# Kernel optimization log

Hardware: AMD Instinct MI355X
Metric: run time of the kernel (lower is better)

## Reference

```python
import jax, jax.numpy as jnp
import numpy as np

CHEB_K = 2  # chebyshev polynomial order (support_ks = [I, A] for cheb_k=2)


def _fc(x, w1, b1, w2, b2, w3, b3):
    # FC module: Linear -> sigmoid -> Linear -> sigmoid -> Linear
    h = jax.nn.sigmoid(x @ w1 + b1)
    h = jax.nn.sigmoid(h @ w2 + b2)
    return h @ w3 + b3


def _preprocess(adj):
    # adj: [B,N,N]; add self-loops then row-normalize
    adj = adj + jnp.eye(adj.shape[-1], dtype=adj.dtype)
    return adj / adj.sum(-1, keepdims=True)


def _gcn(x, adjs, ne, wpool, bpool):
    # x: [B,N,C], adjs: list of [B,N,N], ne: [N,E]
    # wpool: [E, 2*CHEB_K, C, O], bpool: [E, O]
    mats = []
    for A in adjs:
        ks = [jnp.broadcast_to(jnp.eye(A.shape[-1], dtype=A.dtype), A.shape), A]
        for _ in range(2, CHEB_K):
            ks.append(2.0 * jnp.matmul(A, ks[-1]) - ks[-2])
        mats.extend(ks)
    # [B,N,K,C] with K = 2*CHEB_K
    x_g = jnp.stack([jnp.einsum('bnm,bmc->bnc', S, x) for S in mats], axis=2)
    weights = jnp.einsum('nd,dkio->nkio', ne, wpool)  # [N,K,C,O]
    bias = ne @ bpool  # [N,O]
    return jnp.einsum('bnki,nkio->bno', x_g, weights) + bias


def _forward(x, state, ne0, ne1, ne2, fc1_w1, fc1_b1, fc1_w2, fc1_b2, fc1_w3, fc1_b3,
             fc2_w1, fc2_b1, fc2_w2, fc2_b2, fc2_w3, fc2_b3, gate_w, gate_b, upd_w, upd_b):
    hid = upd_w.shape[-1]
    ins = jnp.concatenate([x, state], axis=-1)  # [B,N,dim_in+hid]
    f1 = _fc(ins, fc1_w1, fc1_b1, fc1_w2, fc1_b2, fc1_w3, fc1_b3)  # [B,N,TD]
    f2 = _fc(ins, fc2_w1, fc2_b1, fc2_w2, fc2_b2, fc2_w3, fc2_b3)
    nv1 = jnp.tanh(ne0[:, None, :] * f1)  # einsum 'bd,bnd->bnd' == broadcast mul
    nv2 = jnp.tanh(ne1[:, None, :] * f2)
    adj = jnp.einsum('bnd,bmd->bnm', nv1, nv2) - jnp.einsum('bnd,bmd->bnm', nv2, nv1)
    adj1 = _preprocess(jax.nn.relu(adj))
    adj2 = _preprocess(jax.nn.relu(-jnp.swapaxes(adj, -2, -1)))
    z_r = jax.nn.sigmoid(_gcn(ins, [adj1, adj2], ne2, gate_w, gate_b))
    z, r = z_r[..., :hid], z_r[..., hid:]
    cand = jnp.concatenate([x, z * state], axis=-1)
    hc = jnp.tanh(_gcn(cand, [adj1, adj2], ne2, upd_w, upd_b))
    return r * state + (1.0 - r) * hc


def setup_inputs():
    B, N, DIN, DOUT, ED, TD = 32, 1024, 2, 64, 10, 32
    HG, MID = 16, 2  # hyperGNN_dim, middle_dim hardcoded in FC
    CIN = DIN + DOUT
    K2 = 2 * CHEB_K
    ks = jax.random.split(jax.random.key(0), 16)
    rn = lambda i, shape, s=1.0: jax.random.normal(ks[i], shape, dtype=jnp.float32) * s
    return {
        'x': rn(0, (B, N, DIN)),
        'state': rn(1, (B, N, DOUT)),
        'ne0': rn(2, (B, TD)),
        'ne1': rn(3, (B, TD)),
        'ne2': rn(4, (N, ED), 0.1),
        'fc1_w1': rn(5, (CIN, HG), 0.1), 'fc1_b1': jnp.zeros((HG,), jnp.float32),
        'fc1_w2': rn(6, (HG, MID), 0.1), 'fc1_b2': jnp.zeros((MID,), jnp.float32),
        'fc1_w3': rn(7, (MID, TD), 0.1), 'fc1_b3': jnp.zeros((TD,), jnp.float32),
        'fc2_w1': rn(8, (CIN, HG), 0.1), 'fc2_b1': jnp.zeros((HG,), jnp.float32),
        'fc2_w2': rn(9, (HG, MID), 0.1), 'fc2_b2': jnp.zeros((MID,), jnp.float32),
        'fc2_w3': rn(10, (MID, TD), 0.1), 'fc2_b3': jnp.zeros((TD,), jnp.float32),
        'gate_w': rn(11, (ED, K2, CIN, 2 * DOUT), 0.1),
        'gate_b': rn(12, (ED, 2 * DOUT), 0.1),
        'upd_w': rn(13, (ED, K2, CIN, DOUT), 0.1),
        'upd_b': rn(14, (ED, DOUT), 0.1),
    }


def reference(x, state, ne0, ne1, ne2, fc1_w1, fc1_b1, fc1_w2, fc1_b2, fc1_w3, fc1_b3,
              fc2_w1, fc2_b1, fc2_w2, fc2_b2, fc2_w3, fc2_b3, gate_w, gate_b, upd_w, upd_b):
    return _forward(x, state, ne0, ne1, ne2, fc1_w1, fc1_b1, fc1_w2, fc1_b2, fc1_w3, fc1_b3,
                    fc2_w1, fc2_b1, fc2_w2, fc2_b2, fc2_w3, fc2_b3, gate_w, gate_b, upd_w, upd_b)
```

## Files before the change

kernel.cpp:

```cpp
#include <hip/hip_runtime.h>
#include <math.h>

#define BB   32
#define NN   1024
#define DIN  2
#define DOUT 64
#define CIN  66
#define TD   32
#define ED   10
#define OG   128
#define OU   64
#define KP   160
#define XTR  80
#define PS   88

typedef __bf16 bf16x8 __attribute__((ext_vector_type(8)));
typedef float  f32x4  __attribute__((ext_vector_type(4)));
typedef short  s16x8  __attribute__((ext_vector_type(8)));

__device__ __forceinline__ unsigned short f2b(float f) {
    __bf16 h = (__bf16)f;
    return *(unsigned short*)&h;
}

__global__ __launch_bounds__(256) void k_pre(
    const float* __restrict__ x, const float* __restrict__ state,
    const float* __restrict__ ne0, const float* __restrict__ ne1,
    const float* __restrict__ ne2,
    const float* __restrict__ w11, const float* __restrict__ b11,
    const float* __restrict__ w12, const float* __restrict__ b12,
    const float* __restrict__ w13, const float* __restrict__ b13,
    const float* __restrict__ w21, const float* __restrict__ b21,
    const float* __restrict__ w22, const float* __restrict__ b22,
    const float* __restrict__ w23, const float* __restrict__ b23,
    const float* __restrict__ gate_w, const float* __restrict__ gate_b,
    const float* __restrict__ upd_w, const float* __restrict__ upd_b,
    unsigned short* __restrict__ nv1b, unsigned short* __restrict__ nv2b,
    unsigned short* __restrict__ XT0, unsigned short* __restrict__ XT1,
    unsigned short* __restrict__ BcTg, unsigned short* __restrict__ BcTu,
    float* __restrict__ biasG, float* __restrict__ biasU)
{
    __shared__ float sw[2408];
    __shared__ unsigned short st[68*72];
    int blk = blockIdx.x;
    int t = threadIdx.x;

    if (blk < 128) {
        const int oW1 = 0, oB1 = 1056, oW2 = 1072, oB2 = 1104, oW3 = 1108, oB3 = 1172, F2 = 1204;
        for (int i = t; i < 1056; i += 256) { sw[oW1+i] = w11[i]; sw[F2+oW1+i] = w21[i]; }
        if (t < 16) { sw[oB1+t] = b11[t]; sw[F2+oB1+t] = b21[t]; }
        if (t < 32) { sw[oW2+t] = w12[t]; sw[F2+oW2+t] = w22[t]; }
        if (t < 2)  { sw[oB2+t] = b12[t]; sw[F2+oB2+t] = b22[t]; }
        if (t < 64) { sw[oW3+t] = w13[t]; sw[F2+oW3+t] = w23[t]; }
        if (t >= 64 && t < 96) { sw[oB3+t-64] = b13[t-64]; sw[F2+oB3+t-64] = b23[t-64]; }
        __syncthreads();

        int p = blk*256 + t;
        int b = p >> 10;

        float h1a[16], h1b[16];
        #pragma unroll
        for (int j = 0; j < 16; ++j) { h1a[j] = sw[oB1+j]; h1b[j] = sw[F2+oB1+j]; }
        for (int i = 0; i < CIN; ++i) {
            float v = (i < DIN) ? x[(size_t)p*DIN + i] : state[(size_t)p*DOUT + (i-DIN)];
            #pragma unroll
            for (int jq = 0; jq < 4; ++jq) {
                float4 wa = *(const float4*)&sw[oW1 + i*16 + jq*4];
                float4 wb = *(const float4*)&sw[F2 + oW1 + i*16 + jq*4];
                h1a[jq*4+0] += v*wa.x; h1a[jq*4+1] += v*wa.y;
                h1a[jq*4+2] += v*wa.z; h1a[jq*4+3] += v*wa.w;
                h1b[jq*4+0] += v*wb.x; h1b[jq*4+1] += v*wb.y;
                h1b[jq*4+2] += v*wb.z; h1b[jq*4+3] += v*wb.w;
            }
        }
        #pragma unroll
        for (int j = 0; j < 16; ++j) {
            h1a[j] = 1.f/(1.f + __expf(-h1a[j]));
            h1b[j] = 1.f/(1.f + __expf(-h1b[j]));
        }
        float h2a0 = sw[oB2+0], h2a1 = sw[oB2+1];
        float h2b0 = sw[F2+oB2+0], h2b1 = sw[F2+oB2+1];
        #pragma unroll
        for (int i = 0; i < 16; ++i) {
            h2a0 += h1a[i]*sw[oW2 + i*2 + 0];
            h2a1 += h1a[i]*sw[oW2 + i*2 + 1];
            h2b0 += h1b[i]*sw[F2+oW2 + i*2 + 0];
            h2b1 += h1b[i]*sw[F2+oW2 + i*2 + 1];
        }
        h2a0 = 1.f/(1.f + __expf(-h2a0)); h2a1 = 1.f/(1.f + __expf(-h2a1));
        h2b0 = 1.f/(1.f + __expf(-h2b0)); h2b1 = 1.f/(1.f + __expf(-h2b1));

        const float* pn0 = ne0 + b*TD;
        const float* pn1 = ne1 + b*TD;
        #pragma unroll
        for (int jq = 0; jq < 8; ++jq) {
            float4 ba  = *(const float4*)&sw[oB3 + jq*4];
            float4 wa0 = *(const float4*)&sw[oW3 + jq*4];
            float4 wa1 = *(const float4*)&sw[oW3 + 32 + jq*4];
            float4 bb2 = *(const float4*)&sw[F2+oB3 + jq*4];
            float4 wb0 = *(const float4*)&sw[F2+oW3 + jq*4];
            float4 wb1 = *(const float4*)&sw[F2+oW3 + 32 + jq*4];
            float4 n0 = *(const float4*)&pn0[jq*4];
            float4 n1 = *(const float4*)&pn1[jq*4];
            ushort4 u1, u2;
            u1.x = f2b(tanhf(n0.x*(ba.x + h2a0*wa0.x + h2a1*wa1.x)));
            u1.y = f2b(tanhf(n0.y*(ba.y + h2a0*wa0.y + h2a1*wa1.y)));
            u1.z = f2b(tanhf(n0.z*(ba.z + h2a0*wa0.z + h2a1*wa1.z)));
            u1.w = f2b(tanhf(n0.w*(ba.w + h2a0*wa0.w + h2a1*wa1.w)));
            u2.x = f2b(tanhf(n1.x*(bb2.x + h2b0*wb0.x + h2b1*wb1.x)));
            u2.y = f2b(tanhf(n1.y*(bb2.y + h2b0*wb0.y + h2b1*wb1.y)));
            u2.z = f2b(tanhf(n1.z*(bb2.z + h2b0*wb0.z + h2b1*wb1.z)));
            u2.w = f2b(tanhf(n1.w*(bb2.w + h2b0*wb0.w + h2b1*wb1.w)));
            *(ushort4*)&nv1b[(size_t)p*TD + jq*4] = u1;
            *(ushort4*)&nv2b[(size_t)p*TD + jq*4] = u2;
        }
    } else if (blk < 640) {
        int idx = blk - 128;
        int b = idx >> 4, m0 = (idx & 15)*64;
        for (int i = t; i < 1024; i += 256) {
            int m = i >> 4, cq = i & 15;
            size_t base = (size_t)b*NN + m0 + m;
            float4 v = *(const float4*)&state[base*DOUT + cq*4];
            st[(2 + cq*4 + 0)*72 + m] = f2b(v.x);
            st[(2 + cq*4 + 1)*72 + m] = f2b(v.y);
            st[(2 + cq*4 + 2)*72 + m] = f2b(v.z);
            st[(2 + cq*4 + 3)*72 + m] = f2b(v.w);
        }
        if (t < 128) {
            int m = t >> 1, c = t & 1;
            st[c*72 + m] = f2b(x[((size_t)b*NN + m0 + m)*DIN + c]);
        }
        __syncthreads();
        const unsigned int ONE2 = 0x3F803F80u;
        for (int i = t; i < XTR*8; i += 256) {
            int c = i >> 3, ch = i & 7;
            uint4 v;
            if (c < 66)      v = *(const uint4*)&st[c*72 + ch*8];
            else if (c == 66) v = make_uint4(ONE2, ONE2, ONE2, ONE2);
            else              v = make_uint4(0, 0, 0, 0);
            *(uint4*)&XT0[((size_t)b*XTR + c)*NN + m0 + ch*8] = v;
            if (c < 2 || c >= 66)
                *(uint4*)&XT1[((size_t)b*XTR + c)*NN + m0 + ch*8] = v;
        }
    } else if (blk < 1840) {
        int tid = (blk - 640)*256 + t;
        int c = tid / KP, k = tid - c*KP;
        const float* pool; int O, cc; unsigned short* dst;
        if (c < 1280) { pool = gate_w; O = OG; cc = c;        dst = BcTg; }
        else          { pool = upd_w;  O = OU; cc = c - 1280; dst = BcTu; }
        int d = cc / O, o = cc - d*O;
        float v = 0.f;
        if (k < 132) {
            int kp = (k < 66) ? 0 : 1;
            int i  = (k < 66) ? k : k - 66;
            v = pool[(size_t)((d*4 + kp)*CIN + i)*O + o]
              + pool[(size_t)((d*4 + kp + 2)*CIN + i)*O + o];
        }
        dst[(size_t)cc*KP + k] = f2b(v);
    } else {
        int i = (blk - 1840)*256 + t;
        int n = i / 192, j = i - n*192;
        float v = 0.f;
        if (j < 128) {
            #pragma unroll
            for (int d = 0; d < ED; ++d) v += ne2[(size_t)n*ED + d]*gate_b[d*OG + j];
            biasG[(size_t)n*OG + j] = v;
        } else {
            int o = j - 128;
            #pragma unroll
            for (int d = 0; d < ED; ++d) v += ne2[(size_t)n*ED + d]*upd_b[d*OU + o];
            biasU[(size_t)n*OU + o] = v;
        }
    }
}

__global__ __launch_bounds__(256) void k_aapply(
    const unsigned short* __restrict__ nv1b, const unsigned short* __restrict__ nv2b,
    const unsigned short* __restrict__ XTg, unsigned short* __restrict__ A)
{
    __shared__ unsigned short s_nv1r[64*40], s_nv2r[64*40];
    __shared__ unsigned short s_nv1c[64*40], s_nv2c[64*40];
    __shared__ unsigned short s_p[64*PS];
    __shared__ unsigned short s_xt[80*72];
    __shared__ float s_rs[64];

    int t = threadIdx.x;
    int id = blockIdx.x;
    int b = id & 31, rbase = (id >> 5)*64;
    int w = t >> 6, lane = t & 63, lq = lane >> 4, ln = lane & 15;

    for (int i = t; i < 512; i += 256) {
        int arr = i >> 8, j = i & 255;
        int node = j >> 2, ch = j & 3;
        const unsigned short* src = (arr ? nv2b : nv1b)
            + ((size_t)b*NN + rbase + node)*TD + ch*8;
        unsigned short* dst = (arr ? s_nv2r : s_nv1r) + node*40 + ch*8;
        *(uint4*)dst = *(const uint4*)src;
    }
    __syncthreads();

    bf16x8 a1 = *(const bf16x8*)&s_nv1r[(16*w + ln)*40 + lq*8];
    s16x8 a2s = *(const s16x8*)&s_nv2r[(16*w + ln)*40 + lq*8];
    const s16x8 sgn = {(short)0x8000,(short)0x8000,(short)0x8000,(short)0x8000,
                       (short)0x8000,(short)0x8000,(short)0x8000,(short)0x8000};
    a2s ^= sgn;
    bf16x8 a2n = (bf16x8)a2s;

    f32x4 acc[5];
    #pragma unroll
    for (int i = 0; i < 5; ++i) acc[i] = (f32x4){0.f,0.f,0.f,0.f};
    const f32x4 zero4 = {0.f,0.f,0.f,0.f};

    for (int mb = 0; mb < NN; mb += 64) {
        __syncthreads();
        for (int i = t; i < 512; i += 256) {
            int arr = i >> 8, j = i & 255;
            int node = j >> 2, ch = j & 3;
            const unsigned short* src = (arr ? nv2b : nv1b)
                + ((size_t)b*NN + mb + node)*TD + ch*8;
            unsigned short* dst = (arr ? s_nv2c : s_nv1c) + node*40 + ch*8;
            *(uint4*)dst = *(const uint4*)src;
        }
        for (int i = t; i < 640; i += 256) {
            int c = i >> 3, ch = i & 7;
            *(uint4*)&s_xt[c*72 + ch*8] =
                *(const uint4*)&XTg[((size_t)b*XTR + c)*NN + mb + ch*8];
        }
        __syncthreads();

        #pragma unroll
        for (int j0t = 0; j0t < 4; ++j0t) {
            int j0 = j0t*16;
            bf16x8 b2 = *(const bf16x8*)&s_nv2c[(j0 + ln)*40 + lq*8];
            bf16x8 b1 = *(const bf16x8*)&s_nv1c[(j0 + ln)*40 + lq*8];
            f32x4 s = __builtin_amdgcn_mfma_f32_16x16x32_bf16(a1,  b2, zero4, 0, 0, 0);
            s       = __builtin_amdgcn_mfma_f32_16x16x32_bf16(a2n, b1, s,     0, 0, 0);
            #pragma unroll
            for (int r = 0; r < 4; ++r) {
                float p = fmaxf(s[r], 0.f);
                *(__bf16*)&s_p[(16*w + lq*4 + r)*PS + j0 + ln] = (__bf16)p;
            }
        }

        bf16x8 pa0 = *(const bf16x8*)&s_p[(16*w + ln)*PS +      lq*8];
        bf16x8 pa1 = *(const bf16x8*)&s_p[(16*w + ln)*PS + 32 + lq*8];
        #pragma unroll
        for (int n0t = 0; n0t < 5; ++n0t) {
            int n0 = n0t*16;
            bf16x8 xb0 = *(const bf16x8*)&s_xt[(n0 + ln)*72 +      lq*8];
            bf16x8 xb1 = *(const bf16x8*)&s_xt[(n0 + ln)*72 + 32 + lq*8];
            acc[n0t] = __builtin_amdgcn_mfma_f32_16x16x32_bf16(pa0, xb0, acc[n0t], 0, 0, 0);
            acc[n0t] = __builtin_amdgcn_mfma_f32_16x16x32_bf16(pa1, xb1, acc[n0t], 0, 0, 0);
        }
    }

    if (ln == 2) {
        #pragma unroll
        for (int r = 0; r < 4; ++r) s_rs[16*w + lq*4 + r] = acc[4][r];
    }
    float rinv[4];
    #pragma unroll
    for (int r = 0; r < 4; ++r) rinv[r] = 1.0f / (1.0f + s_rs[16*w + lq*4 + r]);

    #pragma unroll
    for (int n0t = 0; n0t < 5; ++n0t) {
        int c = n0t*16 + ln;
        if (c < CIN) {
            #pragma unroll
            for (int r = 0; r < 4; ++r) {
                int gr = rbase + 16*w + lq*4 + r;
                size_t rowG = (size_t)b*NN + gr;
                unsigned short xu = XTg[((size_t)b*XTR + c)*NN + gr];
                float xr = (float)(*(const __bf16*)&xu);
                A[rowG*KP + c]      = xu;
                A[rowG*KP + 66 + c] = f2b((acc[n0t][r] + xr) * rinv[r]);
            }
        }
    }
    for (int i = t; i < 64*28; i += 256) {
        int rr = i / 28, cc = 132 + (i - 28*(i/28));
        A[((size_t)b*NN + rbase + rr)*KP + cc] = 0;
    }
}

template<int O, int MODE>
__global__ __launch_bounds__(256) void k_gemm(
    const unsigned short* __restrict__ A, const unsigned short* __restrict__ BcT,
    const float* __restrict__ ne2, const float* __restrict__ biasP,
    const float* __restrict__ state, unsigned short* __restrict__ XT1,
    float* __restrict__ rbuf, float* __restrict__ out)
{
    __shared__ unsigned short s_b[80*168];

    int t = threadIdx.x;
    int w = t >> 6, lane = t & 63, lq = lane >> 4, ln = lane & 15;
    int o0 = blockIdx.y*16;
    int rowBlock = blockIdx.x*128;
    int rowW = rowBlock + w*32;

    f32x4 acc[2][2][5];
    #pragma unroll
    for (int h = 0; h < 2; ++h)
        #pragma unroll
        for (int f = 0; f < 2; ++f)
            #pragma unroll
            for (int c = 0; c < 5; ++c) acc[h][f][c] = (f32x4){0.f,0.f,0.f,0.f};

    #pragma unroll
    for (int h = 0; h < 2; ++h) {
        if (h) __syncthreads();
        for (int i = t; i < 1600; i += 256) {
            int cc = i / 20, kc = i - cc*20;
            int d = h*5 + (cc >> 4), oo = cc & 15;
            *(uint4*)&s_b[cc*168 + kc*8] =
                *(const uint4*)&BcT[(size_t)(d*O + o0 + oo)*KP + kc*8];
        }
        __syncthreads();

        #pragma unroll
        for (int kc = 0; kc < 5; ++kc) {
            bf16x8 af0 = *(const bf16x8*)&A[(size_t)(rowW      + ln)*KP + kc*32 + lq*8];
            bf16x8 af1 = *(const bf16x8*)&A[(size_t)(rowW + 16 + ln)*KP + kc*32 + lq*8];
            #pragma unroll
            for (int ct = 0; ct < 5; ++ct) {
                bf16x8 bf = *(const bf16x8*)&s_b[(ct*16 + ln)*168 + kc*32 + lq*8];
                acc[h][0][ct] = __builtin_amdgcn_mfma_f32_16x16x32_bf16(af0, bf, acc[h][0][ct], 0, 0, 0);
                acc[h][1][ct] = __builtin_amdgcn_mfma_f32_16x16x32_bf16(af1, bf, acc[h][1][ct], 0, 0, 0);
            }
        }
    }

    int o = o0 + ln;
    #pragma unroll
    for (int f = 0; f < 2; ++f) {
        #pragma unroll
        for (int r = 0; r < 4; ++r) {
            int row_l = w*32 + 16*f + lq*4 + r;
            size_t rowG = (size_t)rowBlock + row_l;
            int n = (int)(rowG & (NN - 1));
            int bb = (int)(rowG >> 10);
            const float* nep = &ne2[(size_t)n*ED];
            float val = biasP[(size_t)n*O + o];
            #pragma unroll
            for (int d = 0; d < 5; ++d) val += nep[d]     * acc[0][f][d][r];
            #pragma unroll
            for (int d = 0; d < 5; ++d) val += nep[5 + d] * acc[1][f][d][r];
            if (MODE == 0) {
                float sv = 1.f/(1.f + __expf(-val));
                if (o0 < 64) {
                    float zst = sv * state[rowG*DOUT + o];
                    XT1[((size_t)bb*XTR + 2 + o)*NN + n] = f2b(zst);
                } else {
                    rbuf[rowG*DOUT + (o - 64)] = sv;
                }
            } else {
                float hc = tanhf(val);
                float rg = rbuf[rowG*DOUT + o];
                float st = state[rowG*DOUT + o];
                out[rowG*DOUT + o] = rg*st + (1.f - rg)*hc;
            }
        }
    }
}

extern "C" void kernel_launch(void* const* d_in, const int* in_sizes, int n_in,
                              void* d_out, int out_size, void* d_ws, size_t ws_size,
                              hipStream_t stream)
{
    const float* x      = (const float*)d_in[0];
    const float* state  = (const float*)d_in[1];
    const float* ne0    = (const float*)d_in[2];
    const float* ne1    = (const float*)d_in[3];
    const float* ne2    = (const float*)d_in[4];
    const float* f1w1   = (const float*)d_in[5];
    const float* f1b1   = (const float*)d_in[6];
    const float* f1w2   = (const float*)d_in[7];
    const float* f1b2   = (const float*)d_in[8];
    const float* f1w3   = (const float*)d_in[9];
    const float* f1b3   = (const float*)d_in[10];
    const float* f2w1   = (const float*)d_in[11];
    const float* f2b1   = (const float*)d_in[12];
    const float* f2w2   = (const float*)d_in[13];
    const float* f2b2   = (const float*)d_in[14];
    const float* f2w3   = (const float*)d_in[15];
    const float* f2b3   = (const float*)d_in[16];
    const float* gate_w = (const float*)d_in[17];
    const float* gate_b = (const float*)d_in[18];
    const float* upd_w  = (const float*)d_in[19];
    const float* upd_b  = (const float*)d_in[20];

    unsigned short* nv1b = (unsigned short*)d_ws;
    unsigned short* nv2b = nv1b + (size_t)BB*NN*TD;
    unsigned short* XT0  = nv2b + (size_t)BB*NN*TD;
    unsigned short* XT1  = XT0  + (size_t)BB*XTR*NN;
    unsigned short* A    = XT1  + (size_t)BB*XTR*NN;
    unsigned short* BcTg = A    + (size_t)BB*NN*KP;
    unsigned short* BcTu = BcTg + (size_t)1280*KP;
    float* biasG = (float*)(BcTu + (size_t)640*KP);
    float* biasU = biasG + (size_t)NN*OG;
    float* rbuf  = biasU + (size_t)NN*OU;
    float* out   = (float*)d_out;

    k_pre<<<dim3(2608), 256, 0, stream>>>(x, state, ne0, ne1, ne2,
        f1w1, f1b1, f1w2, f1b2, f1w3, f1b3,
        f2w1, f2b1, f2w2, f2b2, f2w3, f2b3,
        gate_w, gate_b, upd_w, upd_b,
        nv1b, nv2b, XT0, XT1, BcTg, BcTu, biasG, biasU);

    k_aapply<<<dim3(512), 256, 0, stream>>>(nv1b, nv2b, XT0, A);

    k_gemm<OG,0><<<dim3(BB*NN/128, 8), 256, 0, stream>>>(A, BcTg, ne2, biasG,
                                                         state, XT1, rbuf, nullptr);

    k_aapply<<<dim3(512), 256, 0, stream>>>(nv1b, nv2b, XT1, A);

    k_gemm<OU,1><<<dim3(BB*NN/128, 4), 256, 0, stream>>>(A, BcTu, ne2, biasU,
                                                         state, nullptr, rbuf, out);
}
```

Before: 255.0 us.

## Split k_aapply work across 8 waves with 512-thread blocks

Doubles the block size of the adjacency-apply kernel to 512 threads. Pairs of waves share a 16-row group: each wave computes half of the score tiles, and after a barrier each takes a subset of the output column tiles (3 or 2). This is meant to raise parallelism and latency hiding with only 512 blocks on the device, at the cost of an extra __syncthreads per iteration and unbalanced MFMA work between the two waves of a pair.

```diff
diff --git a/kernel.cpp b/kernel.cpp
--- a/kernel.cpp
+++ b/kernel.cpp
@@ -174,7 +174,7 @@
     }
 }
 
-__global__ __launch_bounds__(256) void k_aapply(
+__global__ __launch_bounds__(512) void k_aapply(
     const unsigned short* __restrict__ nv1b, const unsigned short* __restrict__ nv2b,
     const unsigned short* __restrict__ XTg, unsigned short* __restrict__ A)
 {
@@ -188,9 +188,10 @@
     int id = blockIdx.x;
     int b = id & 31, rbase = (id >> 5)*64;
     int w = t >> 6, lane = t & 63, lq = lane >> 4, ln = lane & 15;
-
-    for (int i = t; i < 512; i += 256) {
-        int arr = i >> 8, j = i & 255;
+    int g = w >> 1, sub = w & 1;
+
+    {
+        int arr = t >> 8, j = t & 255;
         int node = j >> 2, ch = j & 3;
         const unsigned short* src = (arr ? nv2b : nv1b)
             + ((size_t)b*NN + rbase + node)*TD + ch*8;
@@ -199,29 +200,29 @@
     }
     __syncthreads();
 
-    bf16x8 a1 = *(const bf16x8*)&s_nv1r[(16*w + ln)*40 + lq*8];
-    s16x8 a2s = *(const s16x8*)&s_nv2r[(16*w + ln)*40 + lq*8];
+    bf16x8 a1 = *(const bf16x8*)&s_nv1r[(16*g + ln)*40 + lq*8];
+    s16x8 a2s = *(const s16x8*)&s_nv2r[(16*g + ln)*40 + lq*8];
     const s16x8 sgn = {(short)0x8000,(short)0x8000,(short)0x8000,(short)0x8000,
                        (short)0x8000,(short)0x8000,(short)0x8000,(short)0x8000};
     a2s ^= sgn;
     bf16x8 a2n = (bf16x8)a2s;
 
-    f32x4 acc[5];
+    f32x4 acc[3];
     #pragma unroll
-    for (int i = 0; i < 5; ++i) acc[i] = (f32x4){0.f,0.f,0.f,0.f};
+    for (int i = 0; i < 3; ++i) acc[i] = (f32x4){0.f,0.f,0.f,0.f};
     const f32x4 zero4 = {0.f,0.f,0.f,0.f};
 
     for (int mb = 0; mb < NN; mb += 64) {
         __syncthreads();
-        for (int i = t; i < 512; i += 256) {
-            int arr = i >> 8, j = i & 255;
+        {
+            int arr = t >> 8, j = t & 255;
             int node = j >> 2, ch = j & 3;
             const unsigned short* src = (arr ? nv2b : nv1b)
                 + ((size_t)b*NN + mb + node)*TD + ch*8;
             unsigned short* dst = (arr ? s_nv2c : s_nv1c) + node*40 + ch*8;
             *(uint4*)dst = *(const uint4*)src;
         }
-        for (int i = t; i < 640; i += 256) {
+        for (int i = t; i < 640; i += 512) {
             int c = i >> 3, ch = i & 7;
             *(uint4*)&s_xt[c*72 + ch*8] =
                 *(const uint4*)&XTg[((size_t)b*XTR + c)*NN + mb + ch*8];
@@ -229,8 +230,8 @@
         __syncthreads();
 
         #pragma unroll
-        for (int j0t = 0; j0t < 4; ++j0t) {
-            int j0 = j0t*16;
+        for (int jj = 0; jj < 2; ++jj) {
+            int j0 = (sub*2 + jj)*16;
             bf16x8 b2 = *(const bf16x8*)&s_nv2c[(j0 + ln)*40 + lq*8];
             bf16x8 b1 = *(const bf16x8*)&s_nv1c[(j0 + ln)*40 + lq*8];
             f32x4 s = __builtin_amdgcn_mfma_f32_16x16x32_bf16(a1,  b2, zero4, 0, 0, 0);
@@ -238,46 +239,59 @@
             #pragma unroll
             for (int r = 0; r < 4; ++r) {
                 float p = fmaxf(s[r], 0.f);
-                *(__bf16*)&s_p[(16*w + lq*4 + r)*PS + j0 + ln] = (__bf16)p;
-            }
-        }
-
-        bf16x8 pa0 = *(const bf16x8*)&s_p[(16*w + ln)*PS +      lq*8];
-        bf16x8 pa1 = *(const bf16x8*)&s_p[(16*w + ln)*PS + 32 + lq*8];
-        #pragma unroll
-        for (int n0t = 0; n0t < 5; ++n0t) {
-            int n0 = n0t*16;
-            bf16x8 xb0 = *(const bf16x8*)&s_xt[(n0 + ln)*72 +      lq*8];
-            bf16x8 xb1 = *(const bf16x8*)&s_xt[(n0 + ln)*72 + 32 + lq*8];
-            acc[n0t] = __builtin_amdgcn_mfma_f32_16x16x32_bf16(pa0, xb0, acc[n0t], 0, 0, 0);
-            acc[n0t] = __builtin_amdgcn_mfma_f32_16x16x32_bf16(pa1, xb1, acc[n0t], 0, 0, 0);
-        }
-    }
-
-    if (ln == 2) {
-        #pragma unroll
-        for (int r = 0; r < 4; ++r) s_rs[16*w + lq*4 + r] = acc[4][r];
-    }
+                *(__bf16*)&s_p[(16*g + lq*4 + r)*PS + j0 + ln] = (__bf16)p;
+            }
+        }
+        __syncthreads();
+
+        bf16x8 pa0 = *(const bf16x8*)&s_p[(16*g + ln)*PS +      lq*8];
+        bf16x8 pa1 = *(const bf16x8*)&s_p[(16*g + ln)*PS + 32 + lq*8];
+        if (sub == 0) {
+            #pragma unroll
+            for (int k = 0; k < 3; ++k) {
+                int n0 = k*16;
+                bf16x8 xb0 = *(const bf16x8*)&s_xt[(n0 + ln)*72 +      lq*8];
+                bf16x8 xb1 = *(const bf16x8*)&s_xt[(n0 + ln)*72 + 32 + lq*8];
+                acc[k] = __builtin_amdgcn_mfma_f32_16x16x32_bf16(pa0, xb0, acc[k], 0, 0, 0);
+                acc[k] = __builtin_amdgcn_mfma_f32_16x16x32_bf16(pa1, xb1, acc[k], 0, 0, 0);
+            }
+        } else {
+            #pragma unroll
+            for (int k = 0; k < 2; ++k) {
+                int n0 = (3 + k)*16;
+                bf16x8 xb0 = *(const bf16x8*)&s_xt[(n0 + ln)*72 +      lq*8];
+                bf16x8 xb1 = *(const bf16x8*)&s_xt[(n0 + ln)*72 + 32 + lq*8];
+                acc[k] = __builtin_amdgcn_mfma_f32_16x16x32_bf16(pa0, xb0, acc[k], 0, 0, 0);
+                acc[k] = __builtin_amdgcn_mfma_f32_16x16x32_bf16(pa1, xb1, acc[k], 0, 0, 0);
+            }
+        }
+    }
+
+    if (sub == 1 && ln == 2) {
+        #pragma unroll
+        for (int r = 0; r < 4; ++r) s_rs[16*g + lq*4 + r] = acc[1][r];
+    }
+    __syncthreads();
     float rinv[4];
     #pragma unroll
-    for (int r = 0; r < 4; ++r) rinv[r] = 1.0f / (1.0f + s_rs[16*w + lq*4 + r]);
-
-    #pragma unroll
-    for (int n0t = 0; n0t < 5; ++n0t) {
-        int c = n0t*16 + ln;
+    for (int r = 0; r < 4; ++r) rinv[r] = 1.0f / (1.0f + s_rs[16*g + lq*4 + r]);
+
+    int kmax = sub ? 2 : 3;
+    for (int k = 0; k < kmax; ++k) {
+        int c = (sub ? (3 + k) : k)*16 + ln;
         if (c < CIN) {
             #pragma unroll
             for (int r = 0; r < 4; ++r) {
-                int gr = rbase + 16*w + lq*4 + r;
+                int gr = rbase + 16*g + lq*4 + r;
                 size_t rowG = (size_t)b*NN + gr;
                 unsigned short xu = XTg[((size_t)b*XTR + c)*NN + gr];
                 float xr = (float)(*(const __bf16*)&xu);
                 A[rowG*KP + c]      = xu;
-                A[rowG*KP + 66 + c] = f2b((acc[n0t][r] + xr) * rinv[r]);
-            }
-        }
-    }
-    for (int i = t; i < 64*28; i += 256) {
+                A[rowG*KP + 66 + c] = f2b((acc[k][r] + xr) * rinv[r]);
+            }
+        }
+    }
+    for (int i = t; i < 64*28; i += 512) {
         int rr = i / 28, cc = 132 + (i - 28*(i/28));
         A[((size_t)b*NN + rbase + rr)*KP + cc] = 0;
     }
@@ -407,12 +421,12 @@
         gate_w, gate_b, upd_w, upd_b,
         nv1b, nv2b, XT0, XT1, BcTg, BcTu, biasG, biasU);
 
-    k_aapply<<<dim3(512), 256, 0, stream>>>(nv1b, nv2b, XT0, A);
+    k_aapply<<<dim3(512), 512, 0, stream>>>(nv1b, nv2b, XT0, A);
 
     k_gemm<OG,0><<<dim3(BB*NN/128, 8), 256, 0, stream>>>(A, BcTg, ne2, biasG,
                                                          state, XT1, rbuf, nullptr);
 
-    k_aapply<<<dim3(512), 256, 0, stream>>>(nv1b, nv2b, XT1, A);
+    k_aapply<<<dim3(512), 512, 0, stream>>>(nv1b, nv2b, XT1, A);
 
     k_gemm<OU,1><<<dim3(BB*NN/128, 4), 256, 0, stream>>>(A, BcTu, ne2, biasU,
                                                          state, nullptr, rbuf, out);
```

Result: faster. 235.7 us (-7.6%).
